# Kernel optimization log

Measured on AMD Instinct MI355X. Metric: run time of the kernel, lower is better.

Reference implementation:

```python
import jax, jax.numpy as jnp
import numpy as np

EMB = 768
HEADS = 4
HEAD_DIM = EMB // HEADS


def setup_inputs() -> dict:
    key = jax.random.key(0)
    ks = jax.random.split(key, 11)
    B, S = 8, 2048
    scale = 1.0 / np.sqrt(EMB)
    inp = {
        "q": jax.random.normal(ks[0], (B, S, EMB), dtype=jnp.float32),
        "k": jax.random.normal(ks[1], (B, S, EMB), dtype=jnp.float32),
        "v": jax.random.normal(ks[2], (B, S, EMB), dtype=jnp.float32),
        "Wq": jax.random.normal(ks[3], (EMB, EMB), dtype=jnp.float32) * scale,
        "bq": jnp.zeros((EMB,), dtype=jnp.float32),
        "Wk": jax.random.normal(ks[4], (EMB, EMB), dtype=jnp.float32) * scale,
        "bk": jnp.zeros((EMB,), dtype=jnp.float32),
        "Wv": jax.random.normal(ks[5], (EMB, EMB), dtype=jnp.float32) * scale,
        "bv": jnp.zeros((EMB,), dtype=jnp.float32),
        "Wo": jax.random.normal(ks[6], (EMB, EMB), dtype=jnp.float32) * scale,
        "bo": jnp.zeros((EMB,), dtype=jnp.float32),
    }
    return inp


def reference(q, k, v, Wq, bq, Wk, bk, Wv, bv, Wo, bo):
    B, S, _ = q.shape
    # Linear projections (torch Linear: x @ W.T + b)
    Q = q @ Wq.T + bq
    K = k @ Wk.T + bk
    V = v @ Wv.T + bv
    # split heads: [B, H, S, Dh]
    def split(x):
        return x.reshape(B, S, HEADS, HEAD_DIM).transpose(0, 2, 1, 3)
    Qh, Kh, Vh = split(Q), split(K), split(V)
    # energy [B, H, S, S]; note: original's mask_fill is a non-inplace no-op, so no masking
    energy = jnp.einsum("bhqd,bhkd->bhqk", Qh, Kh)
    att = jax.nn.softmax(energy / jnp.sqrt(jnp.float32(HEAD_DIM)), axis=-1)
    # dropout p=0 -> identity
    out = jnp.einsum("bhqk,bhkd->bhqd", att, Vh)
    out = out.transpose(0, 2, 1, 3).reshape(B, S, EMB)
    return out @ Wo.T + bo
```

## Files before the change

kernel.cpp:

```cpp
#include <hip/hip_runtime.h>
#include <hip/hip_bf16.h>
#include <cstdint>
#include <cstddef>

#define EMB   768
#define HEADS 4
#define HD    192
#define BATCH 8
#define SEQ   2048
#define MROWS (BATCH * SEQ)

typedef __attribute__((ext_vector_type(8))) short bf16x8;
typedef __attribute__((ext_vector_type(4))) float f32x4;

#define GLOBAL_AS __attribute__((address_space(1)))
#define LDS_AS    __attribute__((address_space(3)))

__device__ __forceinline__ void async16(unsigned short* lds, const unsigned short* g) {
    __builtin_amdgcn_global_load_lds((const GLOBAL_AS void*)g, (LDS_AS void*)lds, 16, 0, 0);
}

__device__ __forceinline__ unsigned short f2bf(float f) {
    union { float f; unsigned int u; } v; v.f = f;
    unsigned int u = v.u;
    unsigned int r = u + 0x7fffu + ((u >> 16) & 1u);
    return (unsigned short)(r >> 16);
}

__device__ __forceinline__ unsigned long long pack4bf(float4 f) {
    union { __hip_bfloat162 h; unsigned int u; } a, b;
    a.h = __float22bfloat162_rn(make_float2(f.x, f.y));
    b.h = __float22bfloat162_rn(make_float2(f.z, f.w));
    return (unsigned long long)a.u | ((unsigned long long)b.u << 32);
}

__device__ __forceinline__ int4 pack8bf(float4 lo, float4 hi) {
    union { unsigned long long u[2]; int4 i; } r;
    r.u[0] = pack4bf(lo);
    r.u[1] = pack4bf(hi);
    return r.i;
}

__device__ __forceinline__ int swz(int colbyte, int row) {
    return colbyte ^ ((row & 7) << 4);
}

__global__ __launch_bounds__(256) void conv_kernel(
    const float* __restrict__ x, unsigned short* __restrict__ y, int n4)
{
    int i = blockIdx.x * 256 + threadIdx.x;
    int stride = gridDim.x * 256;
    for (; i < n4; i += stride) {
        float4 f = ((const float4*)x)[i];
        ((unsigned long long*)y)[i] = pack4bf(f);
    }
}

__global__ __launch_bounds__(256) void conv3_kernel(
    const float* __restrict__ a, const float* __restrict__ b,
    const float* __restrict__ c, unsigned short* __restrict__ y, int n4)
{
    int i = blockIdx.x * 256 + threadIdx.x;
    int stride = gridDim.x * 256;
    for (; i < 3 * n4; i += stride) {
        int sel = i / n4, off = i - sel * n4;
        const float* s = (sel == 0) ? a : (sel == 1) ? b : c;
        float4 f = ((const float4*)s)[off];
        ((unsigned long long*)y)[i] = pack4bf(f);
    }
}

#define GEMM_PROLOG                                                          \
    const int tid  = threadIdx.x;                                            \
    const int wg   = (blockIdx.x & 7) * 96 + (blockIdx.x >> 3);              \
    const int n0   = (wg % 6) * 128;                                         \
    const int m0   = (wg / 6) * 128;                                         \
    const int w    = tid >> 6;                                               \
    const int lane = tid & 63;                                               \
    const int l15  = lane & 15;                                              \
    const int quad = lane >> 4;                                              \
    const int wm   = (w >> 1) * 64;                                          \
    const int wn   = (w & 1) * 64;                                           \
    const int arow = lane >> 2;           \
    const int acol = (lane & 3) * 8;                  \
    f32x4 acc[4][4];                                                         \
    _Pragma("unroll")                                                        \
    for (int a = 0; a < 4; a++)                                              \
        _Pragma("unroll")                                                    \
        for (int b = 0; b < 4; b++) acc[a][b] = (f32x4)0.0f;

#define GEMM_STAGE(buf, Aptr, Bptr, k0)                                      \
    _Pragma("unroll")                                                        \
    for (int j = 0; j < 2; j++) {                                            \
        int r = w * 32 + j * 16 + arow;                                      \
        async16(&Al[(buf) * 4096 + (w * 2 + j) * 512],                       \
                Aptr + (size_t)(m0 + r) * 768 + (k0) + acol);                \
        async16(&Bl[(buf) * 4096 + (w * 2 + j) * 512],                       \
                Bptr + (size_t)(n0 + r) * 768 + (k0) + acol);                \
    }

#define GEMM_COMPUTE(buf)                                                    \
    {                                                                        \
        bf16x8 af[4], bfr[4];                                                \
        _Pragma("unroll")                                                    \
        for (int mi = 0; mi < 4; mi++)                                       \
            af[mi] = *(const bf16x8*)&Al[(buf) * 4096 +                      \
                                         (wm + mi * 16 + l15) * 32 + quad * 8]; \
        _Pragma("unroll")                                                    \
        for (int ni = 0; ni < 4; ni++)                                       \
            bfr[ni] = *(const bf16x8*)&Bl[(buf) * 4096 +                     \
                                          (wn + ni * 16 + l15) * 32 + quad * 8]; \
        _Pragma("unroll")                                                    \
        for (int mi = 0; mi < 4; mi++)                                       \
            _Pragma("unroll")                                                \
            for (int ni = 0; ni < 4; ni++)                                   \
                acc[mi][ni] = __builtin_amdgcn_mfma_f32_16x16x32_bf16(       \
                    af[mi], bfr[ni], acc[mi][ni], 0, 0, 0);                  \
    }

#define GEMM_KLOOP(Aptr, Bptr)                                               \
    GEMM_STAGE(0, Aptr, Bptr, 0)                                             \
    for (int k0 = 0; k0 < 768; k0 += 64) {                                   \
        __syncthreads();                                                     \
        GEMM_STAGE(1, Aptr, Bptr, k0 + 32)                                   \
        GEMM_COMPUTE(0)                                                      \
        __syncthreads();                                                     \
        if (k0 + 64 < 768) { GEMM_STAGE(0, Aptr, Bptr, k0 + 64) }            \
        GEMM_COMPUTE(1)                                                      \
    }

#define PROJ_A_LOAD(k0)                                                      \
    {                                                                        \
        const float* pa = X + (size_t)(m0 + w * 32 + arow) * 768 + (k0) + acol; \
        a0 = *(const float4*)pa;  a1 = *(const float4*)(pa + 4);             \
        a2 = *(const float4*)(pa + 16 * 768);                                \
        a3 = *(const float4*)(pa + 16 * 768 + 4);                            \
    }

#define PROJ_A_WRITE(buf)                                                    \
    {                                                                        \
        *(int4*)&Al[(buf) * 4096 + (w * 2 + 0) * 512 + lane * 8] = pack8bf(a0, a1); \
        *(int4*)&Al[(buf) * 4096 + (w * 2 + 1) * 512 + lane * 8] = pack8bf(a2, a3); \
    }

#define PROJ_B_STAGE(buf, k0)                                                \
    _Pragma("unroll")                                                        \
    for (int j = 0; j < 2; j++) {                                            \
        int r = w * 32 + j * 16 + arow;                                      \
        async16(&Bl[(buf) * 4096 + (w * 2 + j) * 512],                       \
                Wb + (size_t)(n0 + r) * 768 + (k0) + acol);                  \
    }

__global__ __launch_bounds__(256) void projqkv_kernel(
    const float* __restrict__ Xq, const float* __restrict__ Xk,
    const float* __restrict__ Xv,
    const unsigned short* __restrict__ Wall,
    const float* __restrict__ bqp, const float* __restrict__ bkp,
    const float* __restrict__ bvp,
    unsigned short* __restrict__ Qo, unsigned short* __restrict__ Ko,
    unsigned short* __restrict__ Vo)
{
    __shared__ __align__(16) unsigned short smem[16384];
    unsigned short* Al = smem;
    unsigned short* Bl = smem + 8192;

    const int tid  = threadIdx.x;
    const int flat = blockIdx.x;
    const int xcd  = flat & 7;
    const int loc  = flat >> 3;
    const int sel  = loc / 96;
    const int wg   = xcd * 96 + (loc - sel * 96);
    const int n0   = (wg % 6) * 128;
    const int m0   = (wg / 6) * 128;
    const int w    = tid >> 6;
    const int lane = tid & 63;
    const int l15  = lane & 15;
    const int quad = lane >> 4;
    const int wm   = (w >> 1) * 64;
    const int wn   = (w & 1) * 64;
    const int arow = lane >> 2;
    const int acol = (lane & 3) * 8;

    const float* X = (sel == 0) ? Xq : (sel == 1) ? Xk : Xv;
    const unsigned short* Wb = Wall + (size_t)sel * (EMB * EMB);
    const float* bias = (sel == 0) ? bqp : (sel == 1) ? bkp : bvp;
    const float scale = (sel == 0) ? 0.07216878364870323f : 1.0f;

    f32x4 acc[4][4];
#pragma unroll
    for (int a = 0; a < 4; a++)
#pragma unroll
        for (int b = 0; b < 4; b++) acc[a][b] = (f32x4)0.0f;

    float4 a0, a1, a2, a3;

    PROJ_A_LOAD(0)
    PROJ_B_STAGE(0, 0)
    PROJ_A_WRITE(0)

    for (int k0 = 0; k0 < 768; k0 += 64) {
        __syncthreads();
        PROJ_A_LOAD(k0 + 32)
        PROJ_B_STAGE(1, k0 + 32)
        GEMM_COMPUTE(0)
        PROJ_A_WRITE(1)
        __syncthreads();
        bool more = (k0 + 64) < 768;
        if (more) { PROJ_A_LOAD(k0 + 64) PROJ_B_STAGE(0, k0 + 64) }
        GEMM_COMPUTE(1)
        if (more) { PROJ_A_WRITE(0) }
    }

    if (sel < 2) {
        unsigned short* out = (sel == 0) ? Qo : Ko;
        const int b = m0 >> 11;
#pragma unroll
        for (int mi = 0; mi < 4; mi++) {
#pragma unroll
            for (int ni = 0; ni < 4; ni++) {
                int jj = n0 + wn + ni * 16 + l15;
                int h  = jj / HD;
                int d  = jj - h * HD;
                float bj = bias[jj];
#pragma unroll
                for (int r = 0; r < 4; r++) {
                    int i = m0 + wm + mi * 16 + quad * 4 + r;
                    int s = i & (SEQ - 1);
                    out[(size_t)((b * HEADS + h) * SEQ + s) * HD + d] =
                        f2bf((acc[mi][ni][r] + bj) * scale);
                }
            }
        }
    } else {
        __syncthreads();
        unsigned short* Tl = smem;
        const int batch = m0 >> 11;
        const int s0    = m0 & (SEQ - 1);
#pragma unroll
        for (int g = 0; g < 4; g++) {
            if ((w & 1) == (g >> 1)) {
#pragma unroll
                for (int t = 0; t < 2; t++) {
                    int ni = (g & 1) * 2 + t;
                    int jj = n0 + (w & 1) * 64 + ni * 16 + l15;
                    int dl = t * 16 + l15;
                    float bj = bias[jj];
#pragma unroll
                    for (int mi = 0; mi < 4; mi++)
#pragma unroll
                        for (int r = 0; r < 4; r++)
                            Tl[dl * 136 + wm + mi * 16 + quad * 4 + r] =
                                f2bf(acc[mi][ni][r] + bj);
                }
            }
            __syncthreads();
#pragma unroll
            for (int t = 0; t < 2; t++) {
                int u  = tid + t * 256;
                int dl = u >> 4;
                int cg = u & 15;
                int jj = n0 + g * 32 + dl;
                int hh = jj / HD;
                int d  = jj - hh * HD;
                *(int4*)(Vo + ((size_t)((batch * HEADS + hh) * HD + d)) * SEQ + s0 + cg * 8) =
                    *(const int4*)&Tl[dl * 136 + cg * 8];
            }
            __syncthreads();
        }
    }
}

__global__ __launch_bounds__(256) void oproj_kernel(
    const unsigned short* __restrict__ A,
    const unsigned short* __restrict__ Wb,
    const float* __restrict__ bias,
    float* __restrict__ out)
{
    __shared__ __align__(16) unsigned short smem[16384];
    unsigned short* Al = smem;
    unsigned short* Bl = smem + 8192;
    GEMM_PROLOG
    GEMM_KLOOP(A, Wb)

#pragma unroll
    for (int mi = 0; mi < 4; mi++) {
#pragma unroll
        for (int ni = 0; ni < 4; ni++) {
            int jj = n0 + wn + ni * 16 + l15;
            float bj = bias[jj];
#pragma unroll
            for (int r = 0; r < 4; r++) {
                int i = m0 + wm + mi * 16 + quad * 4 + r;
                out[(size_t)i * 768 + jj] = acc[mi][ni][r] + bj;
            }
        }
    }
}

__global__ __launch_bounds__(256, 2) void attn_kernel(
    const unsigned short* __restrict__ Q,
    const unsigned short* __restrict__ K,
    const unsigned short* __restrict__ Vt,
    unsigned short* __restrict__ O)
{
    __shared__ __align__(16) unsigned short Kl[64 * 192];
    __shared__ __align__(16) unsigned short Vl[192 * 64];
    __shared__ __align__(16) unsigned short Pl[4 * 32 * 64];

    const int tid  = threadIdx.x;
    const int w    = tid >> 6;
    const int lane = tid & 63;
    const int l15  = lane & 15;
    const int quad = lane >> 4;
    const int flat = blockIdx.x;
    const int loc  = flat >> 3;
    const int bh   = (flat & 7) * 4 + (loc >> 4);
    const int qt   = loc & 15;
    const int b    = bh >> 2;
    const int h    = bh & 3;
    const size_t kbase = (size_t)bh * SEQ * HD;

    bf16x8 qf[2][6];
    {
        const unsigned short* qp =
            Q + kbase + (size_t)(qt * 128 + w * 32 + l15) * HD + quad * 8;
#pragma unroll
        for (int mg = 0; mg < 2; mg++)
#pragma unroll
            for (int kk = 0; kk < 6; kk++)
                qf[mg][kk] = *(const bf16x8*)(qp + mg * 16 * HD + kk * 32);
    }

#pragma unroll
    for (int i = 0; i < 6; i++) {
        int u = tid + i * 256;
        int row = u / 24, rem = u - row * 24;
        int cgp = rem ^ (row & 7);
        async16(&Kl[(i * 256 + w * 64) * 8],
                K + kbase + (size_t)row * HD + cgp * 8);
    }

    f32x4 oacc[2][12];
#pragma unroll
    for (int mg = 0; mg < 2; mg++)
#pragma unroll
        for (int i = 0; i < 12; i++) oacc[mg][i] = (f32x4)0.0f;
    float lacc[2][4] = {{0.f, 0.f, 0.f, 0.f}, {0.f, 0.f, 0.f, 0.f}};

    for (int kt = 0; kt < SEQ / 64; kt++) {
        __syncthreads();

#pragma unroll
        for (int i = 0; i < 6; i++) {
            int u = tid + i * 256;
            int row = u >> 3;
            int cgp = (u & 7) ^ (row & 7);
            async16(&Vl[(i * 256 + w * 64) * 8],
                    Vt + kbase + (size_t)row * SEQ + kt * 64 + cgp * 8);
        }

        f32x4 sacc[2][4];
#pragma unroll
        for (int mg = 0; mg < 2; mg++)
#pragma unroll
            for (int nj = 0; nj < 4; nj++) sacc[mg][nj] = (f32x4)0.0f;

        __builtin_amdgcn_s_setprio(1);
#pragma unroll
        for (int kk = 0; kk < 6; kk++) {
#pragma unroll
            for (int nj = 0; nj < 4; nj++) {
                int row = nj * 16 + l15;
                bf16x8 bfr = *(const bf16x8*)((const char*)Kl + row * 384 +
                                              swz(kk * 64 + quad * 16, row));
                sacc[0][nj] = __builtin_amdgcn_mfma_f32_16x16x32_bf16(
                    qf[0][kk], bfr, sacc[0][nj], 0, 0, 0);
                sacc[1][nj] = __builtin_amdgcn_mfma_f32_16x16x32_bf16(
                    qf[1][kk], bfr, sacc[1][nj], 0, 0, 0);
            }
        }
        __builtin_amdgcn_s_setprio(0);

        {
            char* pw = (char*)Pl + w * 4096;
#pragma unroll
            for (int mg = 0; mg < 2; mg++)
#pragma unroll
                for (int nj = 0; nj < 4; nj++) {
                    int colb = (nj * 16 + l15) * 2;
#pragma unroll
                    for (int r = 0; r < 4; r++) {
                        float pv = __expf(sacc[mg][nj][r]);
                        lacc[mg][r] += pv;
                        int row = mg * 16 + quad * 4 + r;
                        *(unsigned short*)(pw + row * 128 + swz(colb, row)) = f2bf(pv);
                    }
                }
        }

        __syncthreads();

        {
            int ktn = (kt + 1) & (SEQ / 64 - 1);
#pragma unroll
            for (int i = 0; i < 6; i++) {
                int u = tid + i * 256;
                int row = u / 24, rem = u - row * 24;
                int cgp = rem ^ (row & 7);
                async16(&Kl[(i * 256 + w * 64) * 8],
                        K + kbase + (size_t)(ktn * 64 + row) * HD + cgp * 8);
            }
        }

#pragma unroll
        for (int kk = 0; kk < 2; kk++) {
            const char* pr = (const char*)Pl + w * 4096;
            bf16x8 pa0 = *(const bf16x8*)(pr + l15 * 128 + swz(kk * 64 + quad * 16, l15));
            bf16x8 pa1 = *(const bf16x8*)(pr + (16 + l15) * 128 + swz(kk * 64 + quad * 16, 16 + l15));
            __builtin_amdgcn_s_setprio(1);
#pragma unroll
            for (int nf = 0; nf < 12; nf++) {
                int vrow = nf * 16 + l15;
                bf16x8 vb = *(const bf16x8*)((const char*)Vl + vrow * 128 +
                                             swz(kk * 64 + quad * 16, vrow));
                oacc[0][nf] = __builtin_amdgcn_mfma_f32_16x16x32_bf16(pa0, vb, oacc[0][nf], 0, 0, 0);
                oacc[1][nf] = __builtin_amdgcn_mfma_f32_16x16x32_bf16(pa1, vb, oacc[1][nf], 0, 0, 0);
            }
            __builtin_amdgcn_s_setprio(0);
        }
    }

    float inv[2][4];
#pragma unroll
    for (int mg = 0; mg < 2; mg++)
#pragma unroll
        for (int r = 0; r < 4; r++) {
            float lsum = lacc[mg][r];
#pragma unroll
            for (int off = 1; off < 16; off <<= 1)
                lsum += __shfl_xor(lsum, off, 64);
            inv[mg][r] = 1.0f / lsum;
        }
#pragma unroll
    for (int mg = 0; mg < 2; mg++)
#pragma unroll
        for (int nf = 0; nf < 12; nf++) {
            int col = h * HD + nf * 16 + l15;
#pragma unroll
            for (int r = 0; r < 4; r++) {
                int s = qt * 128 + w * 32 + mg * 16 + quad * 4 + r;
                O[(size_t)(b * SEQ + s) * EMB + col] = f2bf(oacc[mg][nf][r] * inv[mg][r]);
            }
        }
}

extern "C" void kernel_launch(void* const* d_in, const int* in_sizes, int n_in,
                              void* d_out, int out_size, void* d_ws, size_t ws_size,
                              hipStream_t stream)
{
    const float* q  = (const float*)d_in[0];
    const float* k  = (const float*)d_in[1];
    const float* v  = (const float*)d_in[2];
    const float* Wq = (const float*)d_in[3];
    const float* bq = (const float*)d_in[4];
    const float* Wk = (const float*)d_in[5];
    const float* bk = (const float*)d_in[6];
    const float* Wv = (const float*)d_in[7];
    const float* bv = (const float*)d_in[8];
    const float* Wo = (const float*)d_in[9];
    const float* bo = (const float*)d_in[10];
    float* out = (float*)d_out;

    unsigned short* S   = (unsigned short*)d_ws;
    unsigned short* Qb  = S  + (size_t)MROWS * EMB;
    unsigned short* Kb  = Qb + (size_t)MROWS * EMB;
    unsigned short* Vb  = Kb + (size_t)MROWS * EMB;

    const int nw4 = EMB * EMB / 4;
    dim3 pb(256);

    conv3_kernel<<<dim3(1728), pb, 0, stream>>>(Wq, Wk, Wv, S, nw4);
    projqkv_kernel<<<dim3(2304), pb, 0, stream>>>(q, k, v, S, bq, bk, bv,
                                                  Qb, Kb, Vb);
    attn_kernel<<<dim3(512), pb, 0, stream>>>(Qb, Kb, Vb, S);
    conv_kernel<<<dim3(576), pb, 0, stream>>>(Wo, Qb, nw4);
    oproj_kernel<<<dim3(768), pb, 0, stream>>>(S, Qb, bo, out);
}
```

Measured before the change: 482.6 us.

## Double GEMM K-tile to 64 and XOR-swizzle LDS tiles in projection kernels

The QKV and output projection GEMMs now stage 64-wide K slices per buffer instead of 32. This halves the number of barrier-separated iterations. The LDS tiles use a 128-byte row layout with an XOR swizzle on the 16-byte column group, applied to both async DMA loads and the fp32->bf16 A-path writes, to avoid bank conflicts on the MFMA fragment reads. LDS use per block doubles to 64KB, which may limit occupancy.

Result: faster. 452.0 us (-6.3%).

```diff
diff --git a/kernel.cpp b/kernel.cpp
--- a/kernel.cpp
+++ b/kernel.cpp
@@ -81,35 +81,40 @@
     const int quad = lane >> 4;                                              \
     const int wm   = (w >> 1) * 64;                                          \
     const int wn   = (w & 1) * 64;                                           \
-    const int arow = lane >> 2;           \
-    const int acol = (lane & 3) * 8;                  \
+    const int aw8  = w * 8;               \
+    const int ar8  = lane >> 3;               \
+    const int acg  = lane & 7;              \
     f32x4 acc[4][4];                                                         \
     _Pragma("unroll")                                                        \
     for (int a = 0; a < 4; a++)                                              \
         _Pragma("unroll")                                                    \
         for (int b = 0; b < 4; b++) acc[a][b] = (f32x4)0.0f;
 
-#define GEMM_STAGE(buf, Aptr, Bptr, k0)                                      \
+#define STAGE_DMA(dst, buf, Sptr, base, k0)                                  \
     _Pragma("unroll")                                                        \
-    for (int j = 0; j < 2; j++) {                                            \
-        int r = w * 32 + j * 16 + arow;                                      \
-        async16(&Al[(buf) * 4096 + (w * 2 + j) * 512],                       \
-                Aptr + (size_t)(m0 + r) * 768 + (k0) + acol);                \
-        async16(&Bl[(buf) * 4096 + (w * 2 + j) * 512],                       \
-                Bptr + (size_t)(n0 + r) * 768 + (k0) + acol);                \
-    }
-
-#define GEMM_COMPUTE(buf)                                                    \
-    {                                                                        \
+    for (int i = 0; i < 4; i++) {                                            \
+        int row = i * 32 + aw8 + ar8;                                        \
+        int cgp = acg ^ (row & 7);                                           \
+        async16(&dst[(buf) * 8192 + (i * 256 + w * 64) * 8],                 \
+                Sptr + (size_t)(base + row) * 768 + (k0) + cgp * 8);         \
+    }
+
+#define GEMM_COMPUTE_V3(buf)                                                 \
+    _Pragma("unroll")                                                        \
+    for (int kk = 0; kk < 2; kk++) {                                         \
         bf16x8 af[4], bfr[4];                                                \
         _Pragma("unroll")                                                    \
-        for (int mi = 0; mi < 4; mi++)                                       \
-            af[mi] = *(const bf16x8*)&Al[(buf) * 4096 +                      \
-                                         (wm + mi * 16 + l15) * 32 + quad * 8]; \
+        for (int mi = 0; mi < 4; mi++) {                                     \
+            int row = wm + mi * 16 + l15;                                    \
+            af[mi] = *(const bf16x8*)((const char*)Al + (buf) * 16384 +      \
+                         row * 128 + swz(kk * 64 + quad * 16, row));         \
+        }                                                                    \
         _Pragma("unroll")                                                    \
-        for (int ni = 0; ni < 4; ni++)                                       \
-            bfr[ni] = *(const bf16x8*)&Bl[(buf) * 4096 +                     \
-                                          (wn + ni * 16 + l15) * 32 + quad * 8]; \
+        for (int ni = 0; ni < 4; ni++) {                                     \
+            int row = wn + ni * 16 + l15;                                    \
+            bfr[ni] = *(const bf16x8*)((const char*)Bl + (buf) * 16384 +     \
+                          row * 128 + swz(kk * 64 + quad * 16, row));        \
+        }                                                                    \
         _Pragma("unroll")                                                    \
         for (int mi = 0; mi < 4; mi++)                                       \
             _Pragma("unroll")                                                \
@@ -118,37 +123,37 @@
                     af[mi], bfr[ni], acc[mi][ni], 0, 0, 0);                  \
     }
 
-#define GEMM_KLOOP(Aptr, Bptr)                                               \
-    GEMM_STAGE(0, Aptr, Bptr, 0)                                             \
-    for (int k0 = 0; k0 < 768; k0 += 64) {                                   \
+#define GEMM_KLOOP_V3(Aptr, Bptr)                                            \
+    STAGE_DMA(Al, 0, Aptr, m0, 0)                                            \
+    STAGE_DMA(Bl, 0, Bptr, n0, 0)                                            \
+    for (int k0 = 0; k0 < 768; k0 += 128) {                                  \
         __syncthreads();                                                     \
-        GEMM_STAGE(1, Aptr, Bptr, k0 + 32)                                   \
-        GEMM_COMPUTE(0)                                                      \
+        STAGE_DMA(Al, 1, Aptr, m0, k0 + 64)                                  \
+        STAGE_DMA(Bl, 1, Bptr, n0, k0 + 64)                                  \
+        GEMM_COMPUTE_V3(0)                                                   \
         __syncthreads();                                                     \
-        if (k0 + 64 < 768) { GEMM_STAGE(0, Aptr, Bptr, k0 + 64) }            \
-        GEMM_COMPUTE(1)                                                      \
-    }
-
-#define PROJ_A_LOAD(k0)                                                      \
-    {                                                                        \
-        const float* pa = X + (size_t)(m0 + w * 32 + arow) * 768 + (k0) + acol; \
-        a0 = *(const float4*)pa;  a1 = *(const float4*)(pa + 4);             \
-        a2 = *(const float4*)(pa + 16 * 768);                                \
-        a3 = *(const float4*)(pa + 16 * 768 + 4);                            \
-    }
-
-#define PROJ_A_WRITE(buf)                                                    \
-    {                                                                        \
-        *(int4*)&Al[(buf) * 4096 + (w * 2 + 0) * 512 + lane * 8] = pack8bf(a0, a1); \
-        *(int4*)&Al[(buf) * 4096 + (w * 2 + 1) * 512 + lane * 8] = pack8bf(a2, a3); \
-    }
-
-#define PROJ_B_STAGE(buf, k0)                                                \
+        if (k0 + 128 < 768) {                                                \
+            STAGE_DMA(Al, 0, Aptr, m0, k0 + 128)                             \
+            STAGE_DMA(Bl, 0, Bptr, n0, k0 + 128)                             \
+        }                                                                    \
+        GEMM_COMPUTE_V3(1)                                                   \
+    }
+
+#define PROJQKV_A_LOAD(k0)                                                   \
     _Pragma("unroll")                                                        \
-    for (int j = 0; j < 2; j++) {                                            \
-        int r = w * 32 + j * 16 + arow;                                      \
-        async16(&Bl[(buf) * 4096 + (w * 2 + j) * 512],                       \
-                Wb + (size_t)(n0 + r) * 768 + (k0) + acol);                  \
+    for (int i = 0; i < 4; i++) {                                            \
+        int row = i * 32 + aw8 + ar8;                                        \
+        const float* pa = X + (size_t)(m0 + row) * 768 + (k0) + acg * 8;     \
+        av[2 * i]     = *(const float4*)pa;                                  \
+        av[2 * i + 1] = *(const float4*)(pa + 4);                            \
+    }
+
+#define PROJQKV_A_WRITE(buf)                                                 \
+    _Pragma("unroll")                                                        \
+    for (int i = 0; i < 4; i++) {                                            \
+        int row = i * 32 + aw8 + ar8;                                        \
+        *(int4*)((char*)Al + (buf) * 16384 + row * 128 + swz(acg * 16, row)) \
+            = pack8bf(av[2 * i], av[2 * i + 1]);                             \
     }
 
 __global__ __launch_bounds__(256) void projqkv_kernel(
@@ -160,9 +165,9 @@
     unsigned short* __restrict__ Qo, unsigned short* __restrict__ Ko,
     unsigned short* __restrict__ Vo)
 {
-    __shared__ __align__(16) unsigned short smem[16384];
+    __shared__ __align__(16) unsigned short smem[32768];
     unsigned short* Al = smem;
-    unsigned short* Bl = smem + 8192;
+    unsigned short* Bl = smem + 16384;
 
     const int tid  = threadIdx.x;
     const int flat = blockIdx.x;
@@ -178,8 +183,9 @@
     const int quad = lane >> 4;
     const int wm   = (w >> 1) * 64;
     const int wn   = (w & 1) * 64;
-    const int arow = lane >> 2;
-    const int acol = (lane & 3) * 8;
+    const int aw8  = w * 8;
+    const int ar8  = lane >> 3;
+    const int acg  = lane & 7;
 
     const float* X = (sel == 0) ? Xq : (sel == 1) ? Xk : Xv;
     const unsigned short* Wb = Wall + (size_t)sel * (EMB * EMB);
@@ -192,23 +198,26 @@
 #pragma unroll
         for (int b = 0; b < 4; b++) acc[a][b] = (f32x4)0.0f;
 
-    float4 a0, a1, a2, a3;
-
-    PROJ_A_LOAD(0)
-    PROJ_B_STAGE(0, 0)
-    PROJ_A_WRITE(0)
-
-    for (int k0 = 0; k0 < 768; k0 += 64) {
+    float4 av[8];
+
+    PROJQKV_A_LOAD(0)
+    STAGE_DMA(Bl, 0, Wb, n0, 0)
+    PROJQKV_A_WRITE(0)
+
+    for (int k0 = 0; k0 < 768; k0 += 128) {
         __syncthreads();
-        PROJ_A_LOAD(k0 + 32)
-        PROJ_B_STAGE(1, k0 + 32)
-        GEMM_COMPUTE(0)
-        PROJ_A_WRITE(1)
+        PROJQKV_A_LOAD(k0 + 64)
+        STAGE_DMA(Bl, 1, Wb, n0, k0 + 64)
+        GEMM_COMPUTE_V3(0)
+        PROJQKV_A_WRITE(1)
         __syncthreads();
-        bool more = (k0 + 64) < 768;
-        if (more) { PROJ_A_LOAD(k0 + 64) PROJ_B_STAGE(0, k0 + 64) }
-        GEMM_COMPUTE(1)
-        if (more) { PROJ_A_WRITE(0) }
+        bool more = (k0 + 128) < 768;
+        if (more) {
+            PROJQKV_A_LOAD(k0 + 128)
+            STAGE_DMA(Bl, 0, Wb, n0, k0 + 128)
+        }
+        GEMM_COMPUTE_V3(1)
+        if (more) { PROJQKV_A_WRITE(0) }
     }
 
     if (sel < 2) {
@@ -276,11 +285,11 @@
     const float* __restrict__ bias,
     float* __restrict__ out)
 {
-    __shared__ __align__(16) unsigned short smem[16384];
+    __shared__ __align__(16) unsigned short smem[32768];
     unsigned short* Al = smem;
-    unsigned short* Bl = smem + 8192;
+    unsigned short* Bl = smem + 16384;
     GEMM_PROLOG
-    GEMM_KLOOP(A, Wb)
+    GEMM_KLOOP_V3(A, Wb)
 
 #pragma unroll
     for (int mi = 0; mi < 4; mi++) {
```
